# Kernel optimization log

Hardware: AMD Instinct MI355X
Metric: run time of the kernel (lower is better)

The kernel has to match this reference:

```python
import jax, jax.numpy as jnp
import numpy as np

H = 1024     # hidden_size
NH = 16      # num heads
HD = H // NH # head_dim = 64
I = 4096     # intermediate_size
EPS = 1e-6


def rmsnorm(x, w, eps=EPS):
    var = jnp.mean(jnp.square(x), axis=-1, keepdims=True)
    return x * jax.lax.rsqrt(var + eps) * w


def attention(x, ctx, wq, wk, wv, wo):
    # x: [B,S,H], ctx: [B,Skv,H]; weights stored [in,out]
    B, S, _ = x.shape
    Skv = ctx.shape[1]
    q = (x @ wq).reshape(B, S, NH, HD)
    k = (ctx @ wk).reshape(B, Skv, NH, HD)
    v = (ctx @ wv).reshape(B, Skv, NH, HD)
    scores = jnp.einsum('bqhd,bkhd->bhqk', q, k) * (HD ** -0.5)
    attn = jax.nn.softmax(scores.astype(jnp.float32), axis=-1).astype(q.dtype)
    out = jnp.einsum('bhqk,bkhd->bqhd', attn, v).reshape(B, S, NH * HD)
    return out @ wo


def mlp(x, wg, wu, wd):
    return (jax.nn.silu(x @ wg) * (x @ wu)) @ wd


def setup_inputs() -> dict:
    key = jax.random.key(0)
    ks = jax.random.split(key, 16)
    p = lambda k, shape: (jax.random.normal(k, shape, jnp.float32) * 0.02)
    return {
        'hidden_states': jax.random.normal(ks[0], (1, 2048, H), jnp.float32),
        'context': jax.random.normal(ks[1], (1, 2048, H), jnp.float32),
        'sa_norm_w': jnp.ones((H,), jnp.float32),
        'sa_wq': p(ks[2], (H, NH * HD)),
        'sa_wk': p(ks[3], (H, NH * HD)),
        'sa_wv': p(ks[4], (H, NH * HD)),
        'sa_wo': p(ks[5], (NH * HD, H)),
        'ca_norm_w': jnp.ones((H,), jnp.float32),
        'ca_wq': p(ks[6], (H, NH * HD)),
        'ca_wk': p(ks[7], (H, NH * HD)),
        'ca_wv': p(ks[8], (H, NH * HD)),
        'ca_wo': p(ks[9], (NH * HD, H)),
        'mlp_norm_w': jnp.ones((H,), jnp.float32),
        'w_gate': p(ks[10], (H, I)),
        'w_up': p(ks[11], (H, I)),
        'w_down': p(ks[12], (I, H)),
    }


def reference(hidden_states, context, sa_norm_w, sa_wq, sa_wk, sa_wv, sa_wo,
              ca_norm_w, ca_wq, ca_wk, ca_wv, ca_wo,
              mlp_norm_w, w_gate, w_up, w_down):
    # self-attention block
    residual = hidden_states
    h = rmsnorm(hidden_states, sa_norm_w)
    h = residual + attention(h, h, sa_wq, sa_wk, sa_wv, sa_wo)
    # cross-attention block
    residual = h
    hn = rmsnorm(h, ca_norm_w)
    h = residual + attention(hn, context, ca_wq, ca_wk, ca_wv, ca_wo)
    # MLP block
    residual = h
    hn = rmsnorm(h, mlp_norm_w)
    h = residual + mlp(hn, w_gate, w_up, w_down)
    return h
```

## Files before the change

kernel.cpp:

```cpp
#include <hip/hip_runtime.h>

#define H 1024
#define S 2048
#define NH 16
#define HD 64
#define ISZ 4096

typedef __attribute__((ext_vector_type(8))) short s8v;
typedef __attribute__((ext_vector_type(4))) short s4v;
typedef __attribute__((ext_vector_type(4))) float f4v;
typedef __attribute__((ext_vector_type(2))) unsigned u2v;

#define MFMA16 __builtin_amdgcn_mfma_f32_16x16x32_bf16

__device__ __forceinline__ short f2bf(float f) {
    unsigned u = __builtin_bit_cast(unsigned, f);
    unsigned r = (u + 0x7FFFu + ((u >> 16) & 1u)) >> 16;
    return (short)r;
}
__device__ __forceinline__ float bf2f(short s) {
    unsigned u = ((unsigned)(unsigned short)s) << 16;
    return __builtin_bit_cast(float, u);
}
__device__ __forceinline__ float exp2_hw(float x) {
    float r; asm("v_exp_f32 %0, %1" : "=v"(r) : "v"(x)); return r;
}
__device__ __forceinline__ unsigned cvt_pk_bf16(float lo, float hi) {
    unsigned r; asm("v_cvt_pk_bf16_f32 %0, %1, %2" : "=v"(r) : "v"(lo), "v"(hi)); return r;
}

__device__ __forceinline__ void gload_lds16(const short* g, short* l) {
    __builtin_amdgcn_global_load_lds(
        (const __attribute__((address_space(1))) void*)g,
        (__attribute__((address_space(3))) void*)l, 16, 0, 0);
}

struct PreArgs {
    const void* hid; const void* ctx;
    const void* sanw; const void* canw; const void* mlpnw;
    const void* w[11];
    short* hidc; short* ctxc; short* xn;
    short* canw_o; short* mlpnw_o;
    short* wT[11];
    int* flag_out;
};

__device__ __forceinline__ void tr_tile(const void* src, short* dst, int K, int N,
                                        int k0, int n0, int rmul, int roff,
                                        int isbf, float* tile ) {
    int t = threadIdx.x;
    int c = t & 31, r0 = t >> 5;
    if (isbf) {
        const short* s = (const short*)src;
#pragma unroll
        for (int i = 0; i < 4; i++)
            tile[(r0 + i * 8) * 33 + c] = bf2f(s[(k0 + r0 + i * 8) * N + n0 + c]);
    } else {
        const float* s = (const float*)src;
#pragma unroll
        for (int i = 0; i < 4; i++)
            tile[(r0 + i * 8) * 33 + c] = s[(k0 + r0 + i * 8) * N + n0 + c];
    }
    __syncthreads();
#pragma unroll
    for (int i = 0; i < 4; i++)
        dst[((n0 + r0 + i * 8) * rmul + roff) * K + k0 + c] = f2bf(tile[c * 33 + r0 + i * 8]);
}

__global__ __launch_bounds__(256) void preamble_kernel(PreArgs pa) {
    __shared__ float tile[32 * 33];
    __shared__ float red[4];
    int b = blockIdx.x;
    int t = threadIdx.x;
    int isbf = (((const unsigned*)pa.sanw)[0] == 0x3F803F80u);
    if (blockIdx.x == 0 && t == 0) pa.flag_out[0] = isbf;

    if (b < 2048) {
        int row = b;
        float xf[4];
        if (isbf) {
            s4v xv = *(const s4v*)((const short*)pa.hid + row * H + t * 4);
#pragma unroll
            for (int j = 0; j < 4; j++) xf[j] = bf2f(xv[j]);
        } else {
            const float* s = (const float*)pa.hid + row * H + t * 4;
#pragma unroll
            for (int j = 0; j < 4; j++) xf[j] = s[j];
        }
        float ss = 0.f;
        s4v cv;
#pragma unroll
        for (int j = 0; j < 4; j++) { cv[j] = f2bf(xf[j]); xf[j] = bf2f(cv[j]); ss += xf[j] * xf[j]; }
        *(s4v*)(pa.hidc + row * H + t * 4) = cv;
        int lane = t & 63, wid = t >> 6;
#pragma unroll
        for (int off = 32; off >= 1; off >>= 1) ss += __shfl_xor(ss, off);
        if (lane == 0) red[wid] = ss;
        __syncthreads();
        float tot = red[0] + red[1] + red[2] + red[3];
        float scale = rsqrtf(tot * (1.f / (float)H) + 1e-6f);
        float wv[4];
        if (isbf) {
            s4v wq = *(const s4v*)((const short*)pa.sanw + t * 4);
#pragma unroll
            for (int j = 0; j < 4; j++) wv[j] = bf2f(wq[j]);
        } else {
            const float* s = (const float*)pa.sanw + t * 4;
#pragma unroll
            for (int j = 0; j < 4; j++) wv[j] = s[j];
        }
        s4v ov;
#pragma unroll
        for (int j = 0; j < 4; j++) ov[j] = f2bf(xf[j] * scale * wv[j]);
        *(s4v*)(pa.xn + row * H + t * 4) = ov;
        return;
    }
    b -= 2048;
    if (b < 1024) {
        int i8 = b * 2048 + t * 8;
        if (isbf) {
            *(s8v*)(pa.ctxc + i8) = *(const s8v*)((const short*)pa.ctx + i8);
        } else {
            const float* s = (const float*)pa.ctx;
            s8v o;
#pragma unroll
            for (int j = 0; j < 8; j++) o[j] = f2bf(s[i8 + j]);
            *(s8v*)(pa.ctxc + i8) = o;
        }
        return;
    }
    b -= 1024;
    if (b < 2) {
        const void* src = (b == 0) ? pa.canw : pa.mlpnw;
        short* dst = (b == 0) ? pa.canw_o : pa.mlpnw_o;
        if (isbf) { if (t * 4 < H) *(s4v*)(dst + t * 4) = *(const s4v*)((const short*)src + t * 4); }
        else {
            const float* s = (const float*)src;
            s4v o;
#pragma unroll
            for (int j = 0; j < 4; j++) o[j] = f2bf(s[t * 4 + j]);
            *(s4v*)(dst + t * 4) = o;
        }
        return;
    }
    b -= 2;
    if (b < 8 * 1024) {
        int w = b >> 10, tl = b & 1023;
        tr_tile(pa.w[w], pa.wT[w], H, H, (tl & 31) * 32, (tl >> 5) * 32, 1, 0, isbf, tile);
        return;
    }
    b -= 8 * 1024;
    if (b < 2 * 4096) {
        int w = 8 + (b >> 12), tl = b & 4095;
        tr_tile(pa.w[w], pa.wT[8], H, ISZ, (tl & 31) * 32, (tl >> 5) * 32, 2, w - 8, isbf, tile);
        return;
    }
    b -= 2 * 4096;
    {
        tr_tile(pa.w[10], pa.wT[10], ISZ, H, (b & 127) * 32, (b >> 7) * 32, 1, 0, isbf, tile);
    }
}

__global__ __launch_bounds__(256) void rmsnorm_kernel(const short* __restrict__ x,
                                                      const short* __restrict__ w,
                                                      short* __restrict__ out) {
    int row = blockIdx.x;
    int t = threadIdx.x;
    int lane = t & 63, wid = t >> 6;
    const short* xr = x + row * H;

    s4v xv = *(const s4v*)(xr + t * 4);
    float xf[4];
    float ss = 0.f;
#pragma unroll
    for (int j = 0; j < 4; j++) { xf[j] = bf2f(xv[j]); ss += xf[j] * xf[j]; }
#pragma unroll
    for (int off = 32; off >= 1; off >>= 1) ss += __shfl_xor(ss, off);

    __shared__ float red[4];
    if (lane == 0) red[wid] = ss;
    __syncthreads();
    float tot = red[0] + red[1] + red[2] + red[3];
    float scale = rsqrtf(tot * (1.f / (float)H) + 1e-6f);

    s4v wv = *(const s4v*)(w + t * 4);
    s4v ov;
#pragma unroll
    for (int j = 0; j < 4; j++) ov[j] = f2bf(xf[j] * scale * bf2f(wv[j]));
    *(s4v*)(out + row * H + t * 4) = ov;
}

template <int BM_, int BN_>
__global__ __launch_bounds__(512, 2) void gemm_bt_kernel(
    const short* __restrict__ A0, const short* __restrict__ A1, int split, int lda,
    const short* __restrict__ Bt,
    void* __restrict__ C, int ldc, int K,
    const short* __restrict__ res,
    const int* __restrict__ dtype_flag,
    short* __restrict__ vtbuf, int vcol0,
    short* __restrict__ silu_out) {

    constexpr int MC = BM_ / 32;
    constexpr int NC = BN_ / 64;
    constexpr int U  = (BM_ + BN_) / 8;
    constexpr int PT = U / 8;
    constexpr int BUF = (BM_ + BN_) * 64;

    __shared__ short lds[2 * BUF];

    const short* A = (blockIdx.y < split) ? A0 : A1;
    int m0 = blockIdx.x * BM_;
    int n0 = blockIdx.y * BN_;

    int t = threadIdx.x;
    int lane = t & 63, wid = t >> 6;
    int quad = lane >> 4, l15 = lane & 15;
    int wr = wid >> 2, wc = wid & 3;
    int ld4 = lane >> 2, lc8 = (lane & 3) * 8;

    f4v acc[MC][NC] = {};

    auto stage = [&](short* buf, int k0) {
#pragma unroll
        for (int s = 0; s < PT; ++s) {
            int u = wid * PT + s;
            if (u < BM_ / 8) {
                int h = u / (BM_ / 16), r16 = u % (BM_ / 16);
                gload_lds16(A + (m0 + r16 * 16 + ld4) * lda + k0 + h * 32 + lc8,
                            buf + h * (BM_ * 32) + r16 * 512);
            } else {
                int ub = u - BM_ / 8;
                int h = ub / (BN_ / 16), r16 = ub % (BN_ / 16);
                gload_lds16(Bt + (n0 + r16 * 16 + ld4) * K + k0 + h * 32 + lc8,
                            buf + BM_ * 64 + h * (BN_ * 32) + r16 * 512);
            }
        }
    };

    auto compute = [&](const short* buf) {
#pragma unroll
        for (int kh = 0; kh < 2; ++kh) {
            s8v af[MC], bfv[NC];
#pragma unroll
            for (int mc = 0; mc < MC; ++mc)
                af[mc] = *(const s8v*)(buf + kh * (BM_ * 32) +
                                       (wr * (BM_ / 2) + mc * 16 + l15) * 32 + quad * 8);
#pragma unroll
            for (int nc = 0; nc < NC; ++nc)
                bfv[nc] = *(const s8v*)(buf + BM_ * 64 + kh * (BN_ * 32) +
                                        (wc * (BN_ / 4) + nc * 16 + l15) * 32 + quad * 8);
#pragma unroll
            for (int mc = 0; mc < MC; ++mc)
#pragma unroll
                for (int nc = 0; nc < NC; ++nc)
                    acc[mc][nc] = MFMA16(af[mc], bfv[nc], acc[mc][nc], 0, 0, 0);
        }
    };

    const int KT = K / 64;
    stage(lds, 0);
    __syncthreads();
    int cur = 0;
    for (int kt = 0; kt < KT - 1; ++kt) {
        stage(lds + (cur ^ 1) * BUF, (kt + 1) * 64);
        compute(lds + cur * BUF);
        __syncthreads();
        cur ^= 1;
    }
    compute(lds + cur * BUF);

    if (silu_out) {
#pragma unroll
        for (int mc = 0; mc < MC; mc++) {
#pragma unroll
            for (int nc = 0; nc < NC; nc++) {
                int row = m0 + wr * (BM_ / 2) + mc * 16 + quad * 4;
                int col = n0 + wc * (BN_ / 4) + nc * 16 + l15;
#pragma unroll
                for (int r = 0; r < 4; r++) {
                    float v = acc[mc][nc][r];
                    float other = __shfl_xor(v, 1);
                    if ((l15 & 1) == 0) {
                        float sig = 1.f / (1.f + __expf(-v));
                        silu_out[(row + r) * ISZ + (col >> 1)] = f2bf(v * sig * other);
                    }
                }
            }
        }
        return;
    }

    int out_fp32 = (dtype_flag != nullptr) && (dtype_flag[0] == 0);

#pragma unroll
    for (int mc = 0; mc < MC; mc++) {
#pragma unroll
        for (int nc = 0; nc < NC; nc++) {
            int row = m0 + wr * (BM_ / 2) + mc * 16 + quad * 4;
            int col = n0 + wc * (BN_ / 4) + nc * 16 + l15;
#pragma unroll
            for (int r = 0; r < 4; r++) {
                float vf = acc[mc][nc][r];
                if (res) vf += bf2f(res[(row + r) * ldc + col]);
                if (vtbuf && col >= vcol0)
                    vtbuf[(col - vcol0) * S + row + r] = f2bf(vf);
                else if (out_fp32)
                    ((float*)C)[(row + r) * ldc + col] = vf;
                else
                    ((short*)C)[(row + r) * ldc + col] = f2bf(vf);
            }
        }
    }
}

__global__ __launch_bounds__(512, 2) void gemm_gu8_kernel(
    const short* __restrict__ A, const short* __restrict__ Bt,
    short* __restrict__ silu_out) {

    __shared__ short lds[65536];

    int lin = blockIdx.x;
    int sw = (lin & 7) * 32 + (lin >> 3);
    int m0 = (sw & 7) * 256;
    int n0 = (sw >> 3) * 256;

    int t = threadIdx.x;
    int lane = t & 63, wid = t >> 6;
    int quad = lane >> 4, l15 = lane & 15;
    int wr = wid >> 2, wc = wid & 3;
    int ld4 = lane >> 2, lc8 = (lane & 3) * 8;

    f4v acc[8][4] = {};

    const short* Arow = A + (m0 + ld4) * 1024 + lc8;
    const short* Brow = Bt + (n0 + ld4) * 1024 + lc8;

    auto stA = [&](int buf, int kt, int kh) {
        short* d = lds + buf * 32768 + kh * 8192;
#pragma unroll
        for (int i = 0; i < 2; i++) {
            int r0 = (wid + 8 * i) * 16;
            gload_lds16(Arow + r0 * 1024 + kt * 64 + kh * 32, d + r0 * 32);
        }
    };
    auto stB = [&](int buf, int kt, int kh) {
        short* d = lds + buf * 32768 + 16384 + kh * 8192;
#pragma unroll
        for (int i = 0; i < 2; i++) {
            int r0 = (wid + 8 * i) * 16;
            gload_lds16(Brow + r0 * 1024 + kt * 64 + kh * 32, d + r0 * 32);
        }
    };

    const int aoff = (wr * 128 + l15) * 32 + quad * 8;
    const int boff = 16384 + (wc * 64 + l15) * 32 + quad * 8;

    stA(0, 0, 0); stB(0, 0, 0); stA(0, 0, 1); stB(0, 0, 1);
    asm volatile("s_waitcnt vmcnt(4)" ::: "memory");
    __builtin_amdgcn_s_barrier();

    int cur = 0;
    for (int kt = 0; kt < 15; ++kt) {
        const short* bc = lds + cur * 32768;
        int nb = cur ^ 1;
        s8v af[8], b0, b1;

#pragma unroll
        for (int mc = 0; mc < 8; ++mc) af[mc] = *(const s8v*)(bc + aoff + mc * 512);
        b0 = *(const s8v*)(bc + boff);
        b1 = *(const s8v*)(bc + boff + 512);
        stA(nb, kt + 1, 0);
        __builtin_amdgcn_s_barrier();
        asm volatile("s_waitcnt lgkmcnt(0)" ::: "memory");
        __builtin_amdgcn_s_setprio(1);
#pragma unroll
        for (int mc = 0; mc < 8; ++mc) {
            acc[mc][0] = MFMA16(af[mc], b0, acc[mc][0], 0, 0, 0);
            acc[mc][1] = MFMA16(af[mc], b1, acc[mc][1], 0, 0, 0);
        }
        __builtin_amdgcn_s_setprio(0);
        __builtin_amdgcn_s_barrier();

        b0 = *(const s8v*)(bc + boff + 1024);
        b1 = *(const s8v*)(bc + boff + 1536);
        stB(nb, kt + 1, 0);
        asm volatile("s_waitcnt vmcnt(4)" ::: "memory");
        __builtin_amdgcn_s_barrier();
        asm volatile("s_waitcnt lgkmcnt(0)" ::: "memory");
        __builtin_amdgcn_s_setprio(1);
#pragma unroll
        for (int mc = 0; mc < 8; ++mc) {
            acc[mc][2] = MFMA16(af[mc], b0, acc[mc][2], 0, 0, 0);
            acc[mc][3] = MFMA16(af[mc], b1, acc[mc][3], 0, 0, 0);
        }
        __builtin_amdgcn_s_setprio(0);
        __builtin_amdgcn_s_barrier();

#pragma unroll
        for (int mc = 0; mc < 8; ++mc) af[mc] = *(const s8v*)(bc + 8192 + aoff + mc * 512);
        b0 = *(const s8v*)(bc + 8192 + boff);
        b1 = *(const s8v*)(bc + 8192 + boff + 512);
        stA(nb, kt + 1, 1);
        __builtin_amdgcn_s_barrier();
        asm volatile("s_waitcnt lgkmcnt(0)" ::: "memory");
        __builtin_amdgcn_s_setprio(1);
#pragma unroll
        for (int mc = 0; mc < 8; ++mc) {
            acc[mc][0] = MFMA16(af[mc], b0, acc[mc][0], 0, 0, 0);
            acc[mc][1] = MFMA16(af[mc], b1, acc[mc][1], 0, 0, 0);
        }
        __builtin_amdgcn_s_setprio(0);
        __builtin_amdgcn_s_barrier();

        b0 = *(const s8v*)(bc + 8192 + boff + 1024);
        b1 = *(const s8v*)(bc + 8192 + boff + 1536);
        stB(nb, kt + 1, 1);
        asm volatile("s_waitcnt vmcnt(4)" ::: "memory");
        __builtin_amdgcn_s_barrier();
        asm volatile("s_waitcnt lgkmcnt(0)" ::: "memory");
        __builtin_amdgcn_s_setprio(1);
#pragma unroll
        for (int mc = 0; mc < 8; ++mc) {
            acc[mc][2] = MFMA16(af[mc], b0, acc[mc][2], 0, 0, 0);
            acc[mc][3] = MFMA16(af[mc], b1, acc[mc][3], 0, 0, 0);
        }
        __builtin_amdgcn_s_setprio(0);
        __builtin_amdgcn_s_barrier();

        cur ^= 1;
    }

    asm volatile("s_waitcnt vmcnt(0)" ::: "memory");
    __builtin_amdgcn_s_barrier();
    {
        const short* bc = lds + cur * 32768;
#pragma unroll
        for (int kh = 0; kh < 2; ++kh) {
            s8v af[8], bv[4];
#pragma unroll
            for (int mc = 0; mc < 8; ++mc) af[mc] = *(const s8v*)(bc + kh * 8192 + aoff + mc * 512);
#pragma unroll
            for (int nc = 0; nc < 4; ++nc) bv[nc] = *(const s8v*)(bc + kh * 8192 + boff + nc * 512);
#pragma unroll
            for (int mc = 0; mc < 8; ++mc)
#pragma unroll
                for (int nc = 0; nc < 4; ++nc)
                    acc[mc][nc] = MFMA16(af[mc], bv[nc], acc[mc][nc], 0, 0, 0);
        }
    }

#pragma unroll
    for (int mc = 0; mc < 8; mc++) {
#pragma unroll
        for (int nc = 0; nc < 4; nc++) {
            int row = m0 + wr * 128 + mc * 16 + quad * 4;
            int col = n0 + wc * 64 + nc * 16 + l15;
#pragma unroll
            for (int r = 0; r < 4; r++) {
                float v = acc[mc][nc][r];
                float other = __shfl_xor(v, 1);
                if ((l15 & 1) == 0) {
                    float sig = 1.f / (1.f + __expf(-v));
                    silu_out[(row + r) * ISZ + (col >> 1)] = f2bf(v * sig * other);
                }
            }
        }
    }
}

__global__ __launch_bounds__(512, 4) void flash_attn_kernel(const short* __restrict__ q,
                                                            const short* __restrict__ kk,
                                                            const short* __restrict__ vt,
                                                            int rs,
                                                            short* __restrict__ o) {
    __shared__ short lds[40960];

    int h = blockIdx.y;
    int q0 = blockIdx.x * 64;
    int t = threadIdx.x;
    int lane = t & 63, wid = t >> 6;
    int quad = lane >> 4, l15 = lane & 15;
    int gw = wid & 3, gh = wid >> 2;
    int kvbase = gh * 1024;
    int kro = l15 & 7;

    int lrow = lane >> 3;
    int lsrc = ((lane & 7) ^ lrow) * 8;

    auto stageKV = [&](int buf, int tt) {
        int kvt = kvbase + tt * 64;
        short* kb = lds + (gh * 2 + buf) * 4096;
        short* vb = lds + 16384 + (gh * 2 + buf) * 4096;
#pragma unroll
        for (int i = 0; i < 2; i++) {
            int r0 = gw * 16 + i * 8;
            gload_lds16(kk + (kvt + r0 + lrow) * rs + h * HD + lsrc, kb + r0 * 64);
            gload_lds16(vt + (h * HD + r0 + lrow) * S + kvt + lsrc, vb + r0 * 64);
        }
    };

    const float qscale = 0.125f * 1.44269504f;
    s8v bq[2];
    int qrow = q0 + gw * 16 + l15;
#pragma unroll
    for (int c = 0; c < 2; c++) {
        s8v raw = *(const s8v*)(q + qrow * rs + h * HD + c * 32 + quad * 8);
#pragma unroll
        for (int j = 0; j < 8; j++) bq[c][j] = f2bf(qscale * bf2f(raw[j]));
    }

    f4v o_acc[4] = {};
    float m_s = -INFINITY, l_s = 0.f;
    short* pw = lds + 32768 + wid * 1024;

    const int NT = 16;
    stageKV(0, 0);
    __syncthreads();
    int cur = 0;
    for (int tt = 0; tt < NT; ++tt) {
        if (tt + 1 < NT) stageKV(cur ^ 1, tt + 1);
        const short* kb = lds + (gh * 2 + cur) * 4096;
        const short* vb = lds + 16384 + (gh * 2 + cur) * 4096;

        f4v st[4];
#pragma unroll
        for (int kc = 0; kc < 4; kc++) {
            f4v a_ = (f4v){0.f, 0.f, 0.f, 0.f};
#pragma unroll
            for (int dc = 0; dc < 2; dc++) {
                s8v kf = *(const s8v*)(kb + (kc * 16 + l15) * 64 + ((dc * 4 + quad) ^ kro) * 8);
                a_ = MFMA16(kf, bq[dc], a_, 0, 0, 0);
            }
            st[kc] = a_;
        }

        float mloc = -INFINITY;
#pragma unroll
        for (int kc = 0; kc < 4; kc++)
#pragma unroll
            for (int r = 0; r < 4; r++) mloc = fmaxf(mloc, st[kc][r]);
        mloc = fmaxf(mloc, __shfl_xor(mloc, 16));
        mloc = fmaxf(mloc, __shfl_xor(mloc, 32));
        float m_new = fmaxf(m_s, mloc);
        float alpha = exp2_hw(m_s - m_new);
        float lloc = 0.f;
#pragma unroll
        for (int kc = 0; kc < 4; kc++)
#pragma unroll
            for (int r = 0; r < 4; r++) {
                float p = exp2_hw(st[kc][r] - m_new);
                st[kc][r] = p;
                lloc += p;
            }
        lloc += __shfl_xor(lloc, 16);
        lloc += __shfl_xor(lloc, 32);
        l_s = l_s * alpha + lloc;
        m_s = m_new;
#pragma unroll
        for (int nd = 0; nd < 4; nd++)
#pragma unroll
            for (int r = 0; r < 4; r++) o_acc[nd][r] *= alpha;

#pragma unroll
        for (int kc = 0; kc < 4; kc++) {
            u2v w;
            w[0] = cvt_pk_bf16(st[kc][0], st[kc][1]);
            w[1] = cvt_pk_bf16(st[kc][2], st[kc][3]);
            int pslot = (kc * 2 + (quad >> 1)) ^ kro;
            *(u2v*)(pw + l15 * 64 + pslot * 8 + (quad & 1) * 4) = w;
        }

#pragma unroll
        for (int nd = 0; nd < 4; nd++) {
#pragma unroll
            for (int kc2 = 0; kc2 < 2; kc2++) {
                s8v vf = *(const s8v*)(vb + (nd * 16 + l15) * 64 + ((kc2 * 4 + quad) ^ kro) * 8);
                s8v pf = *(const s8v*)(pw + l15 * 64 + ((kc2 * 4 + quad) ^ kro) * 8);
                o_acc[nd] = MFMA16(vf, pf, o_acc[nd], 0, 0, 0);
            }
        }
        __syncthreads();
        cur ^= 1;
    }

    float* ex = (float*)lds;
    if (gh == 1) {
        int base = (gw * 64 + lane) * 20;
#pragma unroll
        for (int nd = 0; nd < 4; nd++) *(f4v*)(ex + base + nd * 4) = o_acc[nd];
        ex[base + 16] = m_s;
        ex[base + 17] = l_s;
    }
    __syncthreads();
    if (gh == 1) return;

    int base = (wid * 64 + lane) * 20;
    float mB = ex[base + 16], lB = ex[base + 17];
    float M = fmaxf(m_s, mB);
    float a = exp2_hw(m_s - M), bsc = exp2_hw(mB - M);
    float inv = 1.f / (a * l_s + bsc * lB);
#pragma unroll
    for (int nd = 0; nd < 4; nd++) {
        f4v ob = *(const f4v*)(ex + base + nd * 4);
#pragma unroll
        for (int r = 0; r < 4; r++)
            o_acc[nd][r] = (a * o_acc[nd][r] + bsc * ob[r]) * inv;
    }

#pragma unroll
    for (int nd = 0; nd < 4; nd++)
#pragma unroll
        for (int r = 0; r < 4; r++)
            pw[l15 * 64 + nd * 16 + quad * 4 + r] = f2bf(o_acc[nd][r]);

    int qr = lane >> 2, dc2 = (lane & 3) * 16;
    s8v x0 = *(const s8v*)(pw + qr * 64 + dc2);
    s8v x1 = *(const s8v*)(pw + qr * 64 + dc2 + 8);
    short* dst = o + (q0 + wid * 16 + qr) * H + h * HD + dc2;
    *(s8v*)(dst) = x0;
    *(s8v*)(dst + 8) = x1;
}

extern "C" void kernel_launch(void* const* d_in, const int* in_sizes, int n_in,
                              void* d_out, int out_size, void* d_ws, size_t ws_size,
                              hipStream_t stream) {
    const int SH = S * H;
    const int WH = H * H;
    const int WI = H * ISZ;

    int* flag = (int*)d_ws;
    short* base = (short*)d_ws + 16;

    short* hidc   = base;
    short* ctxc   = hidc + SH;
    short* sanw   = ctxc + SH;
    short* canw   = sanw + H;
    short* mlpnw  = canw + H;
    short* saqkvT = mlpnw + H;
    short* sawoT  = saqkvT + 3 * WH;
    short* caqkvT = sawoT + WH;
    short* cawoT  = caqkvT + 3 * WH;
    short* wguT   = cawoT + WH;
    short* wdT    = wguT + 2 * WI;
    short* xn     = wdT + WI;
    short* qkv    = xn + SH;
    short* ao     = qkv + 3 * SH;
    short* h1     = ao + SH;
    short* gu     = qkv;
    short* h2     = qkv + 8 * SH;
    short* vt     = h2 + SH;

    dim3 blk(256);
    dim3 blk2(512);

    PreArgs pa;
    pa.hid = d_in[0]; pa.ctx = d_in[1];
    pa.sanw = d_in[2]; pa.canw = d_in[7]; pa.mlpnw = d_in[12];
    const void* wsrc[11] = {d_in[3], d_in[4], d_in[5], d_in[6],
                            d_in[8], d_in[9], d_in[10], d_in[11],
                            d_in[13], d_in[14], d_in[15]};
    short* wdst[11] = {saqkvT, saqkvT + WH, saqkvT + 2 * WH, sawoT,
                       caqkvT, caqkvT + WH, caqkvT + 2 * WH, cawoT,
                       wguT, wguT , wdT};
    for (int i = 0; i < 11; i++) { pa.w[i] = wsrc[i]; pa.wT[i] = wdst[i]; }
    pa.hidc = hidc; pa.ctxc = ctxc; pa.xn = xn;
    pa.canw_o = canw; pa.mlpnw_o = mlpnw;
    pa.flag_out = flag;
    const int pre_blocks = 2048 + 1024 + 2 + 8 * 1024 + 2 * 4096 + 4096;
    preamble_kernel<<<pre_blocks, blk, 0, stream>>>(pa);

    gemm_bt_kernel<128, 128><<<dim3(S / 128, 3 * H / 128), blk2, 0, stream>>>(
        xn, xn, 24, H, saqkvT, qkv, 3 * H, H, nullptr, nullptr, vt, 2 * H, nullptr);
    flash_attn_kernel<<<dim3(S / 64, NH), blk2, 0, stream>>>(qkv, qkv + H, vt, 3 * H, ao);
    gemm_bt_kernel<64, 128><<<dim3(S / 64, H / 128), blk2, 0, stream>>>(
        ao, ao, 8, H, sawoT, h1, H, H, hidc, nullptr, nullptr, 0, nullptr);

    rmsnorm_kernel<<<S, blk, 0, stream>>>(h1, canw, xn);
    gemm_bt_kernel<128, 128><<<dim3(S / 128, 3 * H / 128), blk2, 0, stream>>>(
        xn, ctxc, 8, H, caqkvT, qkv, 3 * H, H, nullptr, nullptr, vt, 2 * H, nullptr);
    flash_attn_kernel<<<dim3(S / 64, NH), blk2, 0, stream>>>(qkv, qkv + H, vt, 3 * H, ao);
    gemm_bt_kernel<64, 128><<<dim3(S / 64, H / 128), blk2, 0, stream>>>(
        ao, ao, 8, H, cawoT, h2, H, H, h1, nullptr, nullptr, 0, nullptr);

    rmsnorm_kernel<<<S, blk, 0, stream>>>(h2, mlpnw, xn);
    gemm_gu8_kernel<<<dim3(256), blk2, 0, stream>>>(xn, wguT, gu);
    gemm_bt_kernel<64, 128><<<dim3(S / 64, H / 128), blk2, 0, stream>>>(
        gu, gu, 8, ISZ, wdT, d_out, H, ISZ, h2, flag, nullptr, 0, nullptr);
}
```

Baseline: 443.5 us.

## Add 4-stage LDS-pipelined GEMM for output and down projections

Adds a new GEMM kernel that stages A and B tiles into a four-buffer LDS ring via direct global-to-LDS loads, keeping three tiles in flight. Each step waits only on the oldest tile's loads using explicit vmcnt counts, and MFMA runs at raised wave priority. Block indices are swizzled on a 1D grid to improve L2 reuse. It replaces the three 64x128 projection GEMMs (both attention output projections and the MLP down projection), trading more LDS use and a hand-counted wait scheme for better overlap of memory and compute.

```diff
diff --git a/kernel.cpp b/kernel.cpp
--- a/kernel.cpp
+++ b/kernel.cpp
@@ -34,6 +34,8 @@
         (const __attribute__((address_space(1))) void*)g,
         (__attribute__((address_space(3))) void*)l, 16, 0, 0);
 }
+
+template <int N> struct VMt { static constexpr int val = N; };
 
 struct PreArgs {
     const void* hid; const void* ctx;
@@ -305,6 +307,116 @@
                 if (vtbuf && col >= vcol0)
                     vtbuf[(col - vcol0) * S + row + r] = f2bf(vf);
                 else if (out_fp32)
+                    ((float*)C)[(row + r) * ldc + col] = vf;
+                else
+                    ((short*)C)[(row + r) * ldc + col] = f2bf(vf);
+            }
+        }
+    }
+}
+
+template <int BM_, int BN_>
+__global__ __launch_bounds__(512, 2) void gemm_np_kernel(
+    const short* __restrict__ A, int lda,
+    const short* __restrict__ Bt,
+    void* __restrict__ C, int ldc, int K,
+    const short* __restrict__ res,
+    const int* __restrict__ dtype_flag) {
+
+    constexpr int MC = BM_ / 32;
+    constexpr int NC = BN_ / 64;
+    constexpr int PT = (BM_ + BN_) / 64;
+    constexpr int BUF = (BM_ + BN_) * 64;
+
+    __shared__ short lds[4 * BUF];
+
+    int lin = blockIdx.x;
+    int sw = (lin & 7) * 32 + (lin >> 3);
+    int m0 = (sw & 31) * BM_;
+    int n0 = (sw >> 5) * BN_;
+
+    int t_ = threadIdx.x;
+    int lane = t_ & 63, wid = t_ >> 6;
+    int quad = lane >> 4, l15 = lane & 15;
+    int wr = wid >> 2, wc = wid & 3;
+    int ld4 = lane >> 2, lc8 = (lane & 3) * 8;
+
+    f4v acc[MC][NC] = {};
+
+    auto stage = [&](int bi, int kt) {
+        short* buf = lds + bi * BUF;
+        int k0 = kt * 64;
+#pragma unroll
+        for (int s = 0; s < PT; ++s) {
+            int u = wid * PT + s;
+            if (u < BM_ / 8) {
+                int hh = u / (BM_ / 16), r16 = u % (BM_ / 16);
+                gload_lds16(A + (m0 + r16 * 16 + ld4) * lda + k0 + hh * 32 + lc8,
+                            buf + hh * (BM_ * 32) + r16 * 512);
+            } else {
+                int ub = u - BM_ / 8;
+                int hh = ub / (BN_ / 16), r16 = ub % (BN_ / 16);
+                gload_lds16(Bt + (n0 + r16 * 16 + ld4) * K + k0 + hh * 32 + lc8,
+                            buf + BM_ * 64 + hh * (BN_ * 32) + r16 * 512);
+            }
+        }
+    };
+
+    auto tile = [&](int t, auto wt) {
+        constexpr int W = decltype(wt)::val;
+        if constexpr (W == 9)      asm volatile("s_waitcnt vmcnt(9)" ::: "memory");
+        else if constexpr (W == 6) asm volatile("s_waitcnt vmcnt(6)" ::: "memory");
+        else if constexpr (W == 3) asm volatile("s_waitcnt vmcnt(3)" ::: "memory");
+        else                       asm volatile("s_waitcnt vmcnt(0)" ::: "memory");
+        __builtin_amdgcn_s_barrier();
+        const short* bc = lds + (t & 3) * BUF;
+        s8v af[2][MC], bv[2][NC];
+#pragma unroll
+        for (int kh = 0; kh < 2; ++kh) {
+#pragma unroll
+            for (int mc = 0; mc < MC; ++mc)
+                af[kh][mc] = *(const s8v*)(bc + kh * (BM_ * 32) +
+                                           (wr * (BM_ / 2) + mc * 16 + l15) * 32 + quad * 8);
+#pragma unroll
+            for (int nc = 0; nc < NC; ++nc)
+                bv[kh][nc] = *(const s8v*)(bc + BM_ * 64 + kh * (BN_ * 32) +
+                                           (wc * (BN_ / 4) + nc * 16 + l15) * 32 + quad * 8);
+        }
+        asm volatile("s_waitcnt lgkmcnt(0)" ::: "memory");
+        __builtin_amdgcn_s_barrier();
+        __builtin_amdgcn_s_setprio(1);
+#pragma unroll
+        for (int kh = 0; kh < 2; ++kh)
+#pragma unroll
+            for (int mc = 0; mc < MC; ++mc)
+#pragma unroll
+                for (int nc = 0; nc < NC; ++nc)
+                    acc[mc][nc] = MFMA16(af[kh][mc], bv[kh][nc], acc[mc][nc], 0, 0, 0);
+        __builtin_amdgcn_s_setprio(0);
+    };
+
+    const int KT = K / 64;
+    stage(0, 0); stage(1, 1); stage(2, 2);
+    for (int t = 0; t < KT - 3; ++t) {
+        stage((t + 3) & 3, t + 3);
+        tile(t, VMt<9>{});
+    }
+    tile(KT - 3, VMt<6>{});
+    tile(KT - 2, VMt<3>{});
+    tile(KT - 1, VMt<0>{});
+
+    int out_fp32 = (dtype_flag != nullptr) && (dtype_flag[0] == 0);
+#pragma unroll
+    for (int mc = 0; mc < MC; mc++) {
+#pragma unroll
+        for (int nc = 0; nc < NC; nc++) {
+            int row = m0 + wr * (BM_ / 2) + mc * 16 + quad * 4;
+            int col = n0 + wc * (BN_ / 4) + nc * 16 + l15;
+#pragma unroll
+            for (int r = 0; r < 4; r++) {
+                float vf = acc[mc][nc][r];
+                if (res) vf += bf2f(res[(row + r) * ldc + col]);
+                if (out_fp32)
                     ((float*)C)[(row + r) * ldc + col] = vf;
                 else
                     ((short*)C)[(row + r) * ldc + col] = f2bf(vf);
@@ -672,18 +784,18 @@
     gemm_bt_kernel<128, 128><<<dim3(S / 128, 3 * H / 128), blk2, 0, stream>>>(
         xn, xn, 24, H, saqkvT, qkv, 3 * H, H, nullptr, nullptr, vt, 2 * H, nullptr);
     flash_attn_kernel<<<dim3(S / 64, NH), blk2, 0, stream>>>(qkv, qkv + H, vt, 3 * H, ao);
-    gemm_bt_kernel<64, 128><<<dim3(S / 64, H / 128), blk2, 0, stream>>>(
-        ao, ao, 8, H, sawoT, h1, H, H, hidc, nullptr, nullptr, 0, nullptr);
+    gemm_np_kernel<64, 128><<<dim3(256), blk2, 0, stream>>>(
+        ao, H, sawoT, h1, H, H, hidc, nullptr);
 
     rmsnorm_kernel<<<S, blk, 0, stream>>>(h1, canw, xn);
     gemm_bt_kernel<128, 128><<<dim3(S / 128, 3 * H / 128), blk2, 0, stream>>>(
         xn, ctxc, 8, H, caqkvT, qkv, 3 * H, H, nullptr, nullptr, vt, 2 * H, nullptr);
     flash_attn_kernel<<<dim3(S / 64, NH), blk2, 0, stream>>>(qkv, qkv + H, vt, 3 * H, ao);
-    gemm_bt_kernel<64, 128><<<dim3(S / 64, H / 128), blk2, 0, stream>>>(
-        ao, ao, 8, H, cawoT, h2, H, H, h1, nullptr, nullptr, 0, nullptr);
+    gemm_np_kernel<64, 128><<<dim3(256), blk2, 0, stream>>>(
+        ao, H, cawoT, h2, H, H, h1, nullptr);
 
     rmsnorm_kernel<<<S, blk, 0, stream>>>(h2, mlpnw, xn);
     gemm_gu8_kernel<<<dim3(256), blk2, 0, stream>>>(xn, wguT, gu);
-    gemm_bt_kernel<64, 128><<<dim3(S / 64, H / 128), blk2, 0, stream>>>(
-        gu, gu, 8, ISZ, wdT, d_out, H, ISZ, h2, flag, nullptr, 0, nullptr);
-}
+    gemm_np_kernel<64, 128><<<dim3(256), blk2, 0, stream>>>(
+        gu, ISZ, wdT, d_out, H, ISZ, h2, flag);
+}
```

Measured after the change: 427.1 us. -3.7%, faster.
